# Performance work log

Measured on AMD Instinct MI355X. Metric: run time of the kernel, lower is better.

## Reference

```python
import jax, jax.numpy as jnp
import numpy as np

TOP_K = 4
TAU = 1.0  # training-mode temperature
EPS_NORM = 1e-12
EPS_G = 1e-10


def l2_normalize(x, axis=-1):
    sq = jnp.sum(x * x, axis=axis, keepdims=True)
    return x * jax.lax.rsqrt(jnp.maximum(sq, EPS_NORM))


def setup_inputs() -> dict:
    key = jax.random.key(0)
    k1, k2, k3, k4 = jax.random.split(key, 4)
    B, S, D = 256, 196, 1024
    P, L = 512, 8
    x_embed = jax.random.normal(k1, (B, S, D), dtype=jnp.float32)
    prompt = jax.random.normal(k2, (P, L, D), dtype=jnp.float32) * 0.02
    prompt_key = jax.random.normal(k3, (P, D), dtype=jnp.float32) * 0.02
    gumbel_u = jax.random.uniform(k4, (TOP_K, B, P), dtype=jnp.float32)
    return {"x_embed": x_embed, "prompt": prompt, "prompt_key": prompt_key,
            "gumbel_u": gumbel_u}


def reference(x_embed, prompt, prompt_key, gumbel_u):
    # query: mean over sequence dim (embedding_key='mean')  -> [B, D]
    query = jnp.mean(x_embed, axis=1)
    key_n = l2_normalize(prompt_key, axis=1)   # [P, D]
    q_n = l2_normalize(query, axis=1)          # [B, D]
    sim = jnp.matmul(q_n, key_n.T)             # [B, P]

    P = prompt.shape[0]
    cur = sim
    selected = []
    for i in range(TOP_K):
        # Gumbel(0,1) noise from uniform samples
        g = -jnp.log(-jnp.log(gumbel_u[i] + EPS_G) + EPS_G)
        soft = jax.nn.softmax((cur + g) / TAU, axis=-1)      # [B, P]
        hard = jax.nn.one_hot(jnp.argmax(soft, axis=-1), P, dtype=soft.dtype)
        w = soft + jax.lax.stop_gradient(hard - soft)        # straight-through
        # weighted combination over pool -> [B, L, D]
        sel = jnp.einsum('bp,pld->bld', w, prompt)
        selected.append(sel)
        # training-mode mask-out of selected entries
        cur = cur - w * 1000.0
    return jnp.concatenate(selected, axis=1)  # [B, TOP_K*L, D]
```

## Files before the change

kernel.cpp:

```cpp
#include <hip/hip_runtime.h>
#include <hip/hip_bf16.h>
#include <math.h>

#define B   256
#define S   196
#define D   1024
#define P   512
#define L   8
#define TOPK 4

#define SSPLIT 7
#define SCHUNK (S / SSPLIT)

__global__ __launch_bounds__(256) void mean_partial_kernel(
    const float* __restrict__ x, float* __restrict__ part) {
  const int b = blockIdx.x;
  const int j = blockIdx.y;
  const int t = threadIdx.x;
  const float* xb = x + (size_t)b * S * D + (size_t)j * SCHUNK * D + t * 4;

  float4 acc = make_float4(0.f, 0.f, 0.f, 0.f);
#pragma unroll 4
  for (int s = 0; s < SCHUNK; ++s) {
    float4 v = *(const float4*)(xb + (size_t)s * D);
    acc.x += v.x; acc.y += v.y; acc.z += v.z; acc.w += v.w;
  }
  *(float4*)(part + ((size_t)b * SSPLIT + j) * D + t * 4) = acc;
}

__global__ __launch_bounds__(256) void mean_norm_finalize_kernel(
    const float* __restrict__ part, float* __restrict__ qn) {
  const int b = blockIdx.x;
  const int t = threadIdx.x;

  float4 acc = make_float4(0.f, 0.f, 0.f, 0.f);
#pragma unroll
  for (int j = 0; j < SSPLIT; ++j) {
    float4 v = *(const float4*)(part + ((size_t)b * SSPLIT + j) * D + t * 4);
    acc.x += v.x; acc.y += v.y; acc.z += v.z; acc.w += v.w;
  }
  const float inv = 1.0f / (float)S;
  acc.x *= inv; acc.y *= inv; acc.z *= inv; acc.w *= inv;

  float ss = acc.x * acc.x + acc.y * acc.y + acc.z * acc.z + acc.w * acc.w;
  for (int off = 32; off > 0; off >>= 1) ss += __shfl_down(ss, off, 64);
  __shared__ float wsum[4];
  __shared__ float snorm;
  const int lane = t & 63, w = t >> 6;
  if (lane == 0) wsum[w] = ss;
  __syncthreads();
  if (t == 0) {
    float tot = wsum[0] + wsum[1] + wsum[2] + wsum[3];
    snorm = rsqrtf(fmaxf(tot, 1e-12f));
  }
  __syncthreads();
  const float r = snorm;
  float4 o = make_float4(acc.x * r, acc.y * r, acc.z * r, acc.w * r);
  *(float4*)(qn + (size_t)b * D + t * 4) = o;
}

__global__ __launch_bounds__(256) void key_norm_kernel(
    const float* __restrict__ pk, float* __restrict__ kn) {
  const int p = blockIdx.x;
  const int t = threadIdx.x;
  float4 v = *(const float4*)(pk + (size_t)p * D + t * 4);
  float ss = v.x * v.x + v.y * v.y + v.z * v.z + v.w * v.w;
  for (int off = 32; off > 0; off >>= 1) ss += __shfl_down(ss, off, 64);
  __shared__ float wsum[4];
  __shared__ float snorm;
  const int lane = t & 63, w = t >> 6;
  if (lane == 0) wsum[w] = ss;
  __syncthreads();
  if (t == 0) {
    float tot = wsum[0] + wsum[1] + wsum[2] + wsum[3];
    snorm = rsqrtf(fmaxf(tot, 1e-12f));
  }
  __syncthreads();
  const float r = snorm;
  float4 o = make_float4(v.x * r, v.y * r, v.z * r, v.w * r);
  *(float4*)(kn + (size_t)p * D + t * 4) = o;
}

#define KK 16
__global__ __launch_bounds__(256) void sim_kernel(
    const float* __restrict__ qn, const float* __restrict__ kn,
    float* __restrict__ sim) {
  const int b0 = blockIdx.x * 64;
  const int p0 = blockIdx.y * 64;
  const int k0 = blockIdx.z * (D / 8);
  const int t = threadIdx.x;
  const int tx = t & 15;
  const int ty = t >> 4;

  __shared__ float As[KK][68];
  __shared__ float Bs[KK][68];

  float acc[4][4];
#pragma unroll
  for (int i = 0; i < 4; ++i)
#pragma unroll
    for (int j = 0; j < 4; ++j) acc[i][j] = 0.f;

  const int rr = t >> 2;
  const int k4 = (t & 3) * 4;

  for (int kt = 0; kt < D / 8; kt += KK) {
    float4 a = *(const float4*)(qn + (size_t)(b0 + rr) * D + k0 + kt + k4);
    float4 bb = *(const float4*)(kn + (size_t)(p0 + rr) * D + k0 + kt + k4);
    As[k4 + 0][rr] = a.x; As[k4 + 1][rr] = a.y;
    As[k4 + 2][rr] = a.z; As[k4 + 3][rr] = a.w;
    Bs[k4 + 0][rr] = bb.x; Bs[k4 + 1][rr] = bb.y;
    Bs[k4 + 2][rr] = bb.z; Bs[k4 + 3][rr] = bb.w;
    __syncthreads();
#pragma unroll
    for (int kk = 0; kk < KK; ++kk) {
      float4 av = *(const float4*)&As[kk][ty * 4];
      float4 bv = *(const float4*)&Bs[kk][tx * 4];
      acc[0][0] += av.x * bv.x; acc[0][1] += av.x * bv.y;
      acc[0][2] += av.x * bv.z; acc[0][3] += av.x * bv.w;
      acc[1][0] += av.y * bv.x; acc[1][1] += av.y * bv.y;
      acc[1][2] += av.y * bv.z; acc[1][3] += av.y * bv.w;
      acc[2][0] += av.z * bv.x; acc[2][1] += av.z * bv.y;
      acc[2][2] += av.z * bv.z; acc[2][3] += av.z * bv.w;
      acc[3][0] += av.w * bv.x; acc[3][1] += av.w * bv.y;
      acc[3][2] += av.w * bv.z; acc[3][3] += av.w * bv.w;
    }
    __syncthreads();
  }
#pragma unroll
  for (int i = 0; i < 4; ++i)
#pragma unroll
    for (int j = 0; j < 4; ++j)
      atomicAdd(&sim[(size_t)(b0 + ty * 4 + i) * P + p0 + tx * 4 + j],
                acc[i][j]);
}

__global__ __launch_bounds__(256) void select_kernel(
    const float* __restrict__ sim, const float* __restrict__ gu,
    int* __restrict__ idx) {
  const int b = blockIdx.x;
  const int t = threadIdx.x;
  __shared__ float cur[P];
  cur[t] = sim[(size_t)b * P + t];
  cur[t + 256] = sim[(size_t)b * P + t + 256];
  __syncthreads();

  __shared__ float wval[4];
  __shared__ int widx[4];

  for (int i = 0; i < TOPK; ++i) {
    const float* gui = gu + ((size_t)i * B + b) * P;
    float u0 = gui[t];
    float u1 = gui[t + 256];
    float g0 = -logf(-logf(u0 + 1e-10f) + 1e-10f);
    float g1 = -logf(-logf(u1 + 1e-10f) + 1e-10f);
    float v0 = cur[t] + g0;
    float v1 = cur[t + 256] + g1;
    float bv = v0; int bi = t;
    if (v1 > bv) { bv = v1; bi = t + 256; }
    for (int off = 32; off > 0; off >>= 1) {
      float ov = __shfl_down(bv, off, 64);
      int oi = __shfl_down(bi, off, 64);
      if (ov > bv || (ov == bv && oi < bi)) { bv = ov; bi = oi; }
    }
    const int lane = t & 63, w = t >> 6;
    if (lane == 0) { wval[w] = bv; widx[w] = bi; }
    __syncthreads();
    if (t == 0) {
      float bestv = wval[0]; int besti = widx[0];
      for (int k = 1; k < 4; ++k)
        if (wval[k] > bestv || (wval[k] == bestv && widx[k] < besti)) {
          bestv = wval[k]; besti = widx[k];
        }
      idx[i * B + b] = besti;
      cur[besti] -= 1000.0f;
    }
    __syncthreads();
  }
}

__global__ __launch_bounds__(256) void gather_kernel(
    const int* __restrict__ idx, const float* __restrict__ prompt,
    float* __restrict__ out) {
  const int b = blockIdx.x;
  const int i = blockIdx.y;
  const int t = threadIdx.x;
  const int p = idx[i * B + b];
  const float4* src = (const float4*)(prompt + (size_t)p * L * D);
  float4* dst = (float4*)(out + ((size_t)b * (TOPK * L) + i * L) * D);
#pragma unroll
  for (int l = 0; l < L; ++l) {
    dst[l * (D / 4) + t] = src[l * (D / 4) + t];
  }
}

extern "C" void kernel_launch(void* const* d_in, const int* in_sizes, int n_in,
                              void* d_out, int out_size, void* d_ws,
                              size_t ws_size, hipStream_t stream) {
  const float* x_embed    = (const float*)d_in[0];
  const float* prompt     = (const float*)d_in[1];
  const float* prompt_key = (const float*)d_in[2];
  const float* gumbel_u   = (const float*)d_in[3];
  float* out = (float*)d_out;

  float* sim  = (float*)d_ws;
  float* qn   = sim + (size_t)B * P;
  float* kn   = qn + (size_t)B * D;
  int*   idx  = (int*)(kn + (size_t)P * D);
  float* part = (float*)(idx + TOPK * B);

  hipMemsetAsync(sim, 0, (size_t)B * P * sizeof(float), stream);

  mean_partial_kernel<<<dim3(B, SSPLIT), 256, 0, stream>>>(x_embed, part);
  mean_norm_finalize_kernel<<<B, 256, 0, stream>>>(part, qn);
  key_norm_kernel<<<P, 256, 0, stream>>>(prompt_key, kn);
  sim_kernel<<<dim3(B / 64, P / 64, 8), 256, 0, stream>>>(qn, kn, sim);
  select_kernel<<<B, 256, 0, stream>>>(sim, gumbel_u, idx);
  gather_kernel<<<dim3(B, TOPK), 256, 0, stream>>>(idx, prompt, out);
}
```

Before: 354.7 us.

## Fuse norm kernels, replace atomics with split-K partials, fuse select with gather

Merges the query and key normalization kernels into one launch and drops the memset by having the similarity kernel write per-K-split partial tiles instead of accumulating with atomics. The select kernel now sums the partials and copies the chosen prompts directly, which removes the separate gather launch and the index buffer. This cuts launch count and atomic traffic. In exchange the workspace grows and the gather runs on only 256 blocks instead of 1024, which may reduce parallelism on the dominant copy.

```diff
diff --git a/kernel.cpp b/kernel.cpp
--- a/kernel.cpp
+++ b/kernel.cpp
@@ -11,6 +11,7 @@
 
 #define SSPLIT 7
 #define SCHUNK (S / SSPLIT)
+#define KSPLIT 8
 
 __global__ __launch_bounds__(256) void mean_partial_kernel(
     const float* __restrict__ x, float* __restrict__ part) {
@@ -28,19 +29,29 @@
   *(float4*)(part + ((size_t)b * SSPLIT + j) * D + t * 4) = acc;
 }
 
-__global__ __launch_bounds__(256) void mean_norm_finalize_kernel(
-    const float* __restrict__ part, float* __restrict__ qn) {
-  const int b = blockIdx.x;
-  const int t = threadIdx.x;
-
-  float4 acc = make_float4(0.f, 0.f, 0.f, 0.f);
-#pragma unroll
-  for (int j = 0; j < SSPLIT; ++j) {
-    float4 v = *(const float4*)(part + ((size_t)b * SSPLIT + j) * D + t * 4);
-    acc.x += v.x; acc.y += v.y; acc.z += v.z; acc.w += v.w;
-  }
-  const float inv = 1.0f / (float)S;
-  acc.x *= inv; acc.y *= inv; acc.z *= inv; acc.w *= inv;
+__global__ __launch_bounds__(256) void norm_kernel(
+    const float* __restrict__ part, const float* __restrict__ pk,
+    float* __restrict__ qn, float* __restrict__ kn) {
+  const int t = threadIdx.x;
+  float4 acc;
+  float* dst;
+
+  if (blockIdx.x < B) {
+    const int b = blockIdx.x;
+    acc = make_float4(0.f, 0.f, 0.f, 0.f);
+#pragma unroll
+    for (int j = 0; j < SSPLIT; ++j) {
+      float4 v = *(const float4*)(part + ((size_t)b * SSPLIT + j) * D + t * 4);
+      acc.x += v.x; acc.y += v.y; acc.z += v.z; acc.w += v.w;
+    }
+    const float inv = 1.0f / (float)S;
+    acc.x *= inv; acc.y *= inv; acc.z *= inv; acc.w *= inv;
+    dst = qn + (size_t)b * D + t * 4;
+  } else {
+    const int p = blockIdx.x - B;
+    acc = *(const float4*)(pk + (size_t)p * D + t * 4);
+    dst = kn + (size_t)p * D + t * 4;
+  }
 
   float ss = acc.x * acc.x + acc.y * acc.y + acc.z * acc.z + acc.w * acc.w;
   for (int off = 32; off > 0; off >>= 1) ss += __shfl_down(ss, off, 64);
@@ -55,39 +66,17 @@
   }
   __syncthreads();
   const float r = snorm;
-  float4 o = make_float4(acc.x * r, acc.y * r, acc.z * r, acc.w * r);
-  *(float4*)(qn + (size_t)b * D + t * 4) = o;
-}
-
-__global__ __launch_bounds__(256) void key_norm_kernel(
-    const float* __restrict__ pk, float* __restrict__ kn) {
-  const int p = blockIdx.x;
-  const int t = threadIdx.x;
-  float4 v = *(const float4*)(pk + (size_t)p * D + t * 4);
-  float ss = v.x * v.x + v.y * v.y + v.z * v.z + v.w * v.w;
-  for (int off = 32; off > 0; off >>= 1) ss += __shfl_down(ss, off, 64);
-  __shared__ float wsum[4];
-  __shared__ float snorm;
-  const int lane = t & 63, w = t >> 6;
-  if (lane == 0) wsum[w] = ss;
-  __syncthreads();
-  if (t == 0) {
-    float tot = wsum[0] + wsum[1] + wsum[2] + wsum[3];
-    snorm = rsqrtf(fmaxf(tot, 1e-12f));
-  }
-  __syncthreads();
-  const float r = snorm;
-  float4 o = make_float4(v.x * r, v.y * r, v.z * r, v.w * r);
-  *(float4*)(kn + (size_t)p * D + t * 4) = o;
+  *(float4*)dst = make_float4(acc.x * r, acc.y * r, acc.z * r, acc.w * r);
 }
 
 #define KK 16
 __global__ __launch_bounds__(256) void sim_kernel(
     const float* __restrict__ qn, const float* __restrict__ kn,
-    float* __restrict__ sim) {
+    float* __restrict__ simp) {
   const int b0 = blockIdx.x * 64;
   const int p0 = blockIdx.y * 64;
-  const int k0 = blockIdx.z * (D / 8);
+  const int z  = blockIdx.z;
+  const int k0 = z * (D / KSPLIT);
   const int t = threadIdx.x;
   const int tx = t & 15;
   const int ty = t >> 4;
@@ -104,7 +93,7 @@
   const int rr = t >> 2;
   const int k4 = (t & 3) * 4;
 
-  for (int kt = 0; kt < D / 8; kt += KK) {
+  for (int kt = 0; kt < D / KSPLIT; kt += KK) {
     float4 a = *(const float4*)(qn + (size_t)(b0 + rr) * D + k0 + kt + k4);
     float4 bb = *(const float4*)(kn + (size_t)(p0 + rr) * D + k0 + kt + k4);
     As[k4 + 0][rr] = a.x; As[k4 + 1][rr] = a.y;
@@ -131,22 +120,30 @@
   for (int i = 0; i < 4; ++i)
 #pragma unroll
     for (int j = 0; j < 4; ++j)
-      atomicAdd(&sim[(size_t)(b0 + ty * 4 + i) * P + p0 + tx * 4 + j],
-                acc[i][j]);
-}
-
-__global__ __launch_bounds__(256) void select_kernel(
-    const float* __restrict__ sim, const float* __restrict__ gu,
-    int* __restrict__ idx) {
+      simp[((size_t)z * B + b0 + ty * 4 + i) * P + p0 + tx * 4 + j] =
+          acc[i][j];
+}
+
+__global__ __launch_bounds__(256) void select_gather_kernel(
+    const float* __restrict__ simp, const float* __restrict__ gu,
+    const float* __restrict__ prompt, float* __restrict__ out) {
   const int b = blockIdx.x;
   const int t = threadIdx.x;
   __shared__ float cur[P];
-  cur[t] = sim[(size_t)b * P + t];
-  cur[t + 256] = sim[(size_t)b * P + t + 256];
+
+  float c0 = 0.f, c1 = 0.f;
+#pragma unroll
+  for (int z = 0; z < KSPLIT; ++z) {
+    c0 += simp[((size_t)z * B + b) * P + t];
+    c1 += simp[((size_t)z * B + b) * P + t + 256];
+  }
+  cur[t] = c0;
+  cur[t + 256] = c1;
   __syncthreads();
 
   __shared__ float wval[4];
   __shared__ int widx[4];
+  __shared__ int sidx[TOPK];
 
   for (int i = 0; i < TOPK; ++i) {
     const float* gui = gu + ((size_t)i * B + b) * P;
@@ -172,25 +169,21 @@
         if (wval[k] > bestv || (wval[k] == bestv && widx[k] < besti)) {
           bestv = wval[k]; besti = widx[k];
         }
-      idx[i * B + b] = besti;
+      sidx[i] = besti;
       cur[besti] -= 1000.0f;
     }
     __syncthreads();
   }
-}
-
-__global__ __launch_bounds__(256) void gather_kernel(
-    const int* __restrict__ idx, const float* __restrict__ prompt,
-    float* __restrict__ out) {
-  const int b = blockIdx.x;
-  const int i = blockIdx.y;
-  const int t = threadIdx.x;
-  const int p = idx[i * B + b];
-  const float4* src = (const float4*)(prompt + (size_t)p * L * D);
-  float4* dst = (float4*)(out + ((size_t)b * (TOPK * L) + i * L) * D);
-#pragma unroll
-  for (int l = 0; l < L; ++l) {
-    dst[l * (D / 4) + t] = src[l * (D / 4) + t];
+
+#pragma unroll
+  for (int i = 0; i < TOPK; ++i) {
+    const int p = sidx[i];
+    const float4* src = (const float4*)(prompt + (size_t)p * L * D);
+    float4* dst = (float4*)(out + ((size_t)b * (TOPK * L) + i * L) * D);
+#pragma unroll
+    for (int l = 0; l < L; ++l) {
+      dst[l * (D / 4) + t] = src[l * (D / 4) + t];
+    }
   }
 }
 
@@ -203,18 +196,13 @@
   const float* gumbel_u   = (const float*)d_in[3];
   float* out = (float*)d_out;
 
-  float* sim  = (float*)d_ws;
-  float* qn   = sim + (size_t)B * P;
+  float* simp = (float*)d_ws;
+  float* qn   = simp + (size_t)KSPLIT * B * P;
   float* kn   = qn + (size_t)B * D;
-  int*   idx  = (int*)(kn + (size_t)P * D);
-  float* part = (float*)(idx + TOPK * B);
-
-  hipMemsetAsync(sim, 0, (size_t)B * P * sizeof(float), stream);
+  float* part = kn + (size_t)P * D;
 
   mean_partial_kernel<<<dim3(B, SSPLIT), 256, 0, stream>>>(x_embed, part);
-  mean_norm_finalize_kernel<<<B, 256, 0, stream>>>(part, qn);
-  key_norm_kernel<<<P, 256, 0, stream>>>(prompt_key, kn);
-  sim_kernel<<<dim3(B / 64, P / 64, 8), 256, 0, stream>>>(qn, kn, sim);
-  select_kernel<<<B, 256, 0, stream>>>(sim, gumbel_u, idx);
-  gather_kernel<<<dim3(B, TOPK), 256, 0, stream>>>(idx, prompt, out);
-}
+  norm_kernel<<<B + P, 256, 0, stream>>>(part, prompt_key, qn, kn);
+  sim_kernel<<<dim3(B / 64, P / 64, KSPLIT), 256, 0, stream>>>(qn, kn, simp);
+  select_gather_kernel<<<B, 256, 0, stream>>>(simp, gumbel_u, prompt, out);
+}
```

New measurement: 329.4 us. 1.08x faster.
